# Kernel tuning notes

Measured on AMD Instinct MI355X. Metric: run time of the kernel, lower is better.

The kernel has to match this reference:

```python
import jax, jax.numpy as jnp
import numpy as np

B, C, PC, P = 64, 32, 128, 2048
N = B * C * PC          # 262144 graph nodes
E = 2097152             # ~8 edges per node


def _gcn(x, src, dst, n, W, b):
    # PyG GCNConv: add self loops, sym-normalized mean aggregation of x@W
    xw = x @ W
    sl = jnp.arange(n, dtype=src.dtype)
    s = jnp.concatenate([src, sl]); d = jnp.concatenate([dst, sl])
    deg = jax.ops.segment_sum(jnp.ones(d.shape, xw.dtype), d, num_segments=n)
    dinv = jax.lax.rsqrt(deg)  # deg >= 1 thanks to self loops
    norm = dinv[s] * dinv[d]
    return jax.ops.segment_sum(xw[s] * norm[:, None], d, num_segments=n) + b


def _gat(x, src, dst, n, W, a_src, a_dst, b):
    # PyG GATConv (heads=1): self loops, edge softmax over incoming edges
    xw = x @ W
    sl = jnp.arange(n, dtype=src.dtype)
    s = jnp.concatenate([src, sl]); d = jnp.concatenate([dst, sl])
    e = jax.nn.leaky_relu((xw @ a_src)[s] + (xw @ a_dst)[d], 0.2)
    m = jax.ops.segment_max(jax.lax.stop_gradient(e), d, num_segments=n)
    ex = jnp.exp(e - m[d])
    denom = jax.ops.segment_sum(ex, d, num_segments=n)
    alpha = ex / denom[d]
    return jax.ops.segment_sum(xw[s] * alpha[:, None], d, num_segments=n) + b


def _cross_edges(num_cross, batch_size):
    # faithful to get_c_adjacency: every ordered pair (i!=j) appears twice per graph
    ii, jj = np.meshgrid(np.arange(num_cross), np.arange(num_cross), indexing='ij')
    m = ii != jj
    s, d = ii[m], jj[m]
    s2 = np.concatenate([s, d]); d2 = np.concatenate([d, s])
    off = (np.arange(batch_size) * num_cross)[:, None]
    src = (s2[None] + off).reshape(-1)
    dst = (d2[None] + off).reshape(-1)
    return jnp.asarray(src, jnp.int32), jnp.asarray(dst, jnp.int32)


def _conv1d(x, W, b):
    y = jax.lax.conv_general_dilated(x, W, (2,), ((1, 1),), dimension_numbers=('NCH', 'OIH', 'NCH'))
    return y + b[None, :, None]


def _bn_eval(x, gamma, beta):
    # BatchNorm1d in eval mode with default running stats (mean 0, var 1)
    scale = gamma / np.float32(np.sqrt(1.0 + 1e-5))
    return x * scale[None, :, None] + beta[None, :, None]


def setup_inputs() -> dict:
    key = jax.random.key(0)
    ks = jax.random.split(key, 32)
    rn = lambda k, sh, s=0.1: (jax.random.normal(k, sh, jnp.float32) * s)
    return {
        'x': jax.random.normal(ks[0], (N, 19), jnp.float32),
        'edge_index': jax.random.randint(ks[1], (2, E), 0, N, jnp.int32),
        'points': jax.random.normal(ks[2], (B, 3, P), jnp.float32),
        'W1': rn(ks[3], (19, 32)), 'b1': rn(ks[4], (32,)),
        'W2': rn(ks[5], (32, 64)), 'b2': rn(ks[6], (64,)),
        'W3': rn(ks[7], (64, 64)), 'b3': rn(ks[8], (64,)),
        'Wg1': rn(ks[9], (64, 64)), 'asrc1': rn(ks[10], (64,)), 'adst1': rn(ks[11], (64,)), 'bg1': rn(ks[12], (64,)),
        'Wg2': rn(ks[13], (64, 64)), 'asrc2': rn(ks[14], (64,)), 'adst2': rn(ks[15], (64,)), 'bg2': rn(ks[16], (64,)),
        'c1W': rn(ks[17], (32, 3, 3)), 'c1b': rn(ks[18], (32,)),
        'g1': 1.0 + rn(ks[19], (32,)), 'be1': rn(ks[20], (32,)),
        'c2W': rn(ks[21], (64, 32, 3)), 'c2b': rn(ks[22], (64,)),
        'g2': 1.0 + rn(ks[23], (64,)), 'be2': rn(ks[24], (64,)),
        'c3W': rn(ks[25], (64, 64, 3)), 'c3b': rn(ks[26], (64,)),
        'Wl2': rn(ks[27], (64, 64)), 'bl2': rn(ks[28], (64,)),
        'Wl3': rn(ks[29], (64, 1)), 'bl3': rn(ks[30], (1,)),
        'batch_size': B, 'num_cross': C, 'num_pieces': PC,
    }


def reference(x, edge_index, points, W1, b1, W2, b2, W3, b3,
              Wg1, asrc1, adst1, bg1, Wg2, asrc2, adst2, bg2,
              c1W, c1b, g1, be1, c2W, c2b, g2, be2, c3W, c3b,
              Wl2, bl2, Wl3, bl3, batch_size, num_cross, num_pieces):
    src, dst = edge_index[0], edge_index[1]
    n = x.shape[0]
    h = jax.nn.relu(_gcn(x, src, dst, n, W1, b1))  # dropout is a no-op in eval
    h = jax.nn.leaky_relu(_gcn(h, src, dst, n, W2, b2), 0.01)
    h = jax.nn.leaky_relu(_gcn(h, src, dst, n, W3, b3), 0.01)
    h = _gat(h, src, dst, n, Wg1, asrc1, adst1, bg1)
    h = h.reshape(batch_size, num_cross, num_pieces, -1).mean(-2)  # [B, C, 64]
    s2, d2 = _cross_edges(num_cross, batch_size)
    h = _gat(h.reshape(batch_size * num_cross, 64), s2, d2, batch_size * num_cross, Wg2, asrc2, adst2, bg2)
    h = h.reshape(batch_size, num_cross, 64).mean(1)  # [B, 64]
    p = _bn_eval(jax.nn.leaky_relu(_conv1d(points, c1W, c1b), 0.01), g1, be1)
    p = _bn_eval(jax.nn.leaky_relu(_conv1d(p, c2W, c2b), 0.01), g2, be2)
    p = jax.nn.leaky_relu(_conv1d(p, c3W, c3b), 0.01).mean(-1)  # AdaptiveAvgPool1d(1).squeeze -> [B, 64]
    h = h + p
    h = jax.nn.leaky_relu(h @ Wl2 + bl2, 0.01)
    return jax.nn.sigmoid(h @ Wl3 + bl3)  # [B, 1]
```

## Files before the change

### kernel.cpp

```cpp
#include <hip/hip_runtime.h>
#include <cstdint>
#include <cstddef>

#define NN 262144
#define EE 2097152
#define BB 64
#define CCROSS 32
#define PCC 128
#define PP 2048
#define NBUCK 256
#define BCAP 12288

typedef _Float16 f16;
typedef __attribute__((ext_vector_type(2))) _Float16 f16x2;
typedef __attribute__((ext_vector_type(4))) _Float16 f16x4;
typedef __attribute__((ext_vector_type(8))) _Float16 f16x8;
typedef __attribute__((ext_vector_type(4))) float f32x4;

static __device__ __forceinline__ float lrelu(float x, float s) { return x > 0.f ? x : s * x; }

#if __has_builtin(__builtin_amdgcn_fdot2)
static __device__ __forceinline__ float dot2f(unsigned x, unsigned w, float c) {
    return __builtin_amdgcn_fdot2(__builtin_bit_cast(f16x2, x), __builtin_bit_cast(f16x2, w), c, false);
}
#else
static __device__ __forceinline__ float dot2f(unsigned x, unsigned w, float c) {
    f16x2 a = __builtin_bit_cast(f16x2, x);
    f16x2 b = __builtin_bit_cast(f16x2, w);
    return fmaf((float)a[0], (float)b[0], fmaf((float)a[1], (float)b[1], c));
}
#endif

__global__ __launch_bounds__(256) void bucket_a_k(const int* __restrict__ src, const int* __restrict__ dst,
                                                  unsigned* __restrict__ buckets, int* __restrict__ gcnt) {
    __shared__ int hist[NBUCK];
    __shared__ int base[NBUCK];
    __shared__ unsigned short rankbuf[8192];
    const int tid = threadIdx.x;
    const int e0 = blockIdx.x * 8192;
    hist[tid] = 0;
    __syncthreads();
    for (int i = tid; i < 8192; i += 256) {
        int d = dst[e0 + i];
        rankbuf[i] = (unsigned short)atomicAdd(&hist[d >> 10], 1);
    }
    __syncthreads();
    base[tid] = tid * BCAP + atomicAdd(&gcnt[tid], hist[tid]);
    __syncthreads();
    for (int i = tid; i < 8192; i += 256) {
        int s = src[e0 + i];
        int d = dst[e0 + i];
        int b = d >> 10;
        buckets[base[b] + rankbuf[i]] = ((unsigned)s << 10) | (unsigned)(d & 1023);
    }
}

__global__ void bucket_scan_k(const int* __restrict__ gcnt, int* __restrict__ bbase, int* __restrict__ rp) {
    __shared__ int tmp[256];
    int tid = threadIdx.x;
    int v = gcnt[tid];
    tmp[tid] = v;
    __syncthreads();
    for (int off = 1; off < 256; off <<= 1) {
        int t = (tid >= off) ? tmp[tid - off] : 0;
        __syncthreads();
        tmp[tid] += t;
        __syncthreads();
    }
    bbase[tid] = tmp[tid] - v;
    if (tid == 0) rp[NN] = EE;
}

__global__ __launch_bounds__(256) void bucket_b_k(const unsigned* __restrict__ buckets, const int* __restrict__ gcnt,
                                                  const int* __restrict__ bbase, int* __restrict__ rp,
                                                  float* __restrict__ dinv, int* __restrict__ col) {
    __shared__ int cnt[1024];
    __shared__ int scan[1024];
    __shared__ int wsum[256];
    const int b = blockIdx.x;
    const int tid = threadIdx.x;
    int n = gcnt[b];
    if (n > BCAP) n = BCAP;
    const unsigned* eb = buckets + (size_t)b * BCAP;
    const int gb = bbase[b];
    for (int i = tid; i < 1024; i += 256) cnt[i] = 0;
    __syncthreads();
    for (int i = tid; i < n; i += 256) atomicAdd(&cnt[eb[i] & 1023], 1);
    __syncthreads();
    int b4 = tid * 4;
    int c0 = cnt[b4], c1 = cnt[b4 + 1], c2 = cnt[b4 + 2], c3 = cnt[b4 + 3];
    int tsum = c0 + c1 + c2 + c3;
    wsum[tid] = tsum;
    __syncthreads();
    for (int off = 1; off < 256; off <<= 1) {
        int t = (tid >= off) ? wsum[tid - off] : 0;
        __syncthreads();
        wsum[tid] += t;
        __syncthreads();
    }
    int excl = wsum[tid] - tsum;
    scan[b4] = excl;
    scan[b4 + 1] = excl + c0;
    scan[b4 + 2] = excl + c0 + c1;
    scan[b4 + 3] = excl + c0 + c1 + c2;
    int vbase = b * 1024 + b4;
    rp[vbase + 0] = gb + scan[b4 + 0];
    rp[vbase + 1] = gb + scan[b4 + 1];
    rp[vbase + 2] = gb + scan[b4 + 2];
    rp[vbase + 3] = gb + scan[b4 + 3];
    dinv[vbase + 0] = rsqrtf((float)(c0 + 1));
    dinv[vbase + 1] = rsqrtf((float)(c1 + 1));
    dinv[vbase + 2] = rsqrtf((float)(c2 + 1));
    dinv[vbase + 3] = rsqrtf((float)(c3 + 1));
    __syncthreads();
    for (int i = tid; i < 1024; i += 256) cnt[i] = 0;
    __syncthreads();
    for (int i = tid; i < n; i += 256) {
        unsigned p = eb[i];
        int dl = p & 1023;
        int r = atomicAdd(&cnt[dl], 1);
        col[gb + scan[dl] + r] = (int)(p >> 10);
    }
}

__global__ void zprep_k(const float* __restrict__ x, const float* __restrict__ dinv, f16* __restrict__ z) {
    int v = blockIdx.x * 256 + threadIdx.x;
    if (v >= NN) return;
    float dv = dinv[v];
    const float* xr = x + (size_t)v * 19;
    float vv[20];
#pragma unroll
    for (int k = 0; k < 19; k++) vv[k] = dv * xr[k];
    vv[19] = 0.f;
    f16x4* zr = (f16x4*)(z + (size_t)v * 32);
#pragma unroll
    for (int c = 0; c < 5; c++) {
        f16x4 t = {(f16)vv[4 * c], (f16)vv[4 * c + 1], (f16)vv[4 * c + 2], (f16)vv[4 * c + 3]};
        zr[c] = t;
    }
    f16x4 zz = {(f16)0.f, (f16)0.f, (f16)0.f, (f16)0.f};
#pragma unroll
    for (int c = 5; c < 8; c++) zr[c] = zz;
}

#define ZSTR1 36
template <int KINR, int KOUT, int ACT>
__global__ __launch_bounds__(256) void fused_agg_gemm_k(const f16* __restrict__ z, const int* __restrict__ rp,
                                                        const int* __restrict__ col, const float* __restrict__ Wg,
                                                        const float* __restrict__ dinv, const float* __restrict__ bias,
                                                        f16* __restrict__ zout) {
    constexpr int NO = KOUT / 4;
    __shared__ float Wl[32 * KOUT];
    __shared__ float zrow[64 * ZSTR1];
    const int tid = threadIdx.x;
    for (int i = tid; i < 32 * KOUT; i += 256) Wl[i] = (i < KINR * KOUT) ? Wg[i] : 0.f;

    const int r = tid >> 2;
    const int idx = tid & 3;
    const int v = blockIdx.x * 64 + r;
    const f16x8* z8 = (const f16x8*)z;
    f16x8 a = z8[(size_t)v * 4 + idx];
    float acc8[8];
#pragma unroll
    for (int j = 0; j < 8; j++) acc8[j] = (float)a[j];
    int st = rp[v], e = rp[v + 1];
    int i = st;
    for (; i + 4 <= e; i += 4) {
        int u0 = col[i], u1 = col[i + 1], u2 = col[i + 2], u3 = col[i + 3];
        f16x8 a0 = z8[(size_t)u0 * 4 + idx];
        f16x8 a1 = z8[(size_t)u1 * 4 + idx];
        f16x8 a2 = z8[(size_t)u2 * 4 + idx];
        f16x8 a3 = z8[(size_t)u3 * 4 + idx];
#pragma unroll
        for (int j = 0; j < 8; j++)
            acc8[j] += ((float)a0[j] + (float)a1[j]) + ((float)a2[j] + (float)a3[j]);
    }
    for (; i < e; i++) {
        f16x8 aa = z8[(size_t)col[i] * 4 + idx];
#pragma unroll
        for (int j = 0; j < 8; j++) acc8[j] += (float)aa[j];
    }
    float4 s0, s1;
    s0.x = acc8[0]; s0.y = acc8[1]; s0.z = acc8[2]; s0.w = acc8[3];
    s1.x = acc8[4]; s1.y = acc8[5]; s1.z = acc8[6]; s1.w = acc8[7];
    *(float4*)&zrow[r * ZSTR1 + idx * 8] = s0;
    *(float4*)&zrow[r * ZSTR1 + idx * 8 + 4] = s1;
    __syncthreads();

    float acc[NO];
#pragma unroll
    for (int j = 0; j < NO; j++) acc[j] = 0.f;
#pragma unroll 4
    for (int k = 0; k < 32; k++) {
        float zv = zrow[r * ZSTR1 + k];
        const float* wr = Wl + k * KOUT + NO * idx;
#pragma unroll
        for (int j = 0; j < NO; j++) acc[j] = fmaf(zv, wr[j], acc[j]);
    }
    float dv = dinv[v];
    f16 hv[NO];
#pragma unroll
    for (int j = 0; j < NO; j++) {
        float o = dv * acc[j] + bias[NO * idx + j];
        o = (ACT == 0) ? fmaxf(o, 0.f) : lrelu(o, 0.01f);
        hv[j] = (f16)(o * dv);
    }
    if constexpr (NO == 8) {
        f16x8 h = {hv[0], hv[1], hv[2], hv[3], hv[4], hv[5], hv[6], hv[7]};
        *(f16x8*)(zout + (size_t)v * KOUT + NO * idx) = h;
    } else {
        f16x8 h0 = {hv[0], hv[1], hv[2], hv[3], hv[4], hv[5], hv[6], hv[7]};
        f16x8 h1 = {hv[8], hv[9], hv[10], hv[11], hv[12], hv[13], hv[14], hv[15]};
        f16x8* yo = (f16x8*)(zout + (size_t)v * KOUT + NO * idx);
        yo[0] = h0; yo[1] = h1;
    }
}

__global__ void pack_w_k(const float* __restrict__ W, f16* __restrict__ out) {
    int o = blockIdx.x * 256 + threadIdx.x;
    if (o >= 4096) return;
    int frag = o >> 9;
    int kt = frag >> 2;
    int c = frag & 3;
    int idx = o & 511;
    int l = idx >> 3;
    int j = idx & 7;
    int k = kt * 32 + ((l >> 4) << 3) + j;
    int n = 16 * c + (l & 15);
    out[o] = (f16)W[k * 64 + n];
}

__global__ void pack_c2_k(const float* __restrict__ W, f16* __restrict__ out) {
    int o = blockIdx.x * 256 + threadIdx.x;
    if (o >= 64 * 96) return;
    int ch = o / 96, r = o - ch * 96;
    int k = r >> 5, ci = r & 31;
    out[o] = (f16)W[ch * 96 + ci * 3 + k];
}

__global__ void pack_c3_k(const float* __restrict__ W, f16* __restrict__ out) {
    int o = blockIdx.x * 256 + threadIdx.x;
    if (o >= 64 * 192) return;
    int ch = o / 192, r = o - ch * 192;
    int k = r >> 6, ci = r & 63;
    out[o] = (f16)W[ch * 192 + ci * 3 + k];
}

#define HSTR 72
__global__ __launch_bounds__(256) void gemm3_gat_k(const f16* __restrict__ y, const int* __restrict__ rp,
                                                   const int* __restrict__ col, const f16* __restrict__ w3p,
                                                   const float* __restrict__ dinv, const float* __restrict__ b3,
                                                   const f16* __restrict__ wgp, const float* __restrict__ av,
                                                   const float* __restrict__ ad, f16* __restrict__ xw,
                                                   float* __restrict__ es, float* __restrict__ ed) {
    __shared__ f16 zin[64 * HSTR];
    __shared__ f16 hh[64 * HSTR];
    const int tid = threadIdx.x;
    const int v0 = blockIdx.x * 64;
    {
        const int row = tid >> 2;
        const int idx = tid & 3;
        const int v = v0 + row;
        const f16x8* y8 = (const f16x8*)y;
        f16x8 s0 = y8[(size_t)v * 8 + idx * 2];
        f16x8 s1 = y8[(size_t)v * 8 + idx * 2 + 1];
        float acc[16];
#pragma unroll
        for (int j = 0; j < 8; j++) { acc[j] = (float)s0[j]; acc[8 + j] = (float)s1[j]; }
        int s = rp[v], e = rp[v + 1];
        int i = s;
        for (; i + 4 <= e; i += 4) {
            int u0 = col[i], u1 = col[i + 1], u2 = col[i + 2], u3 = col[i + 3];
            f16x8 a0 = y8[(size_t)u0 * 8 + idx * 2];
            f16x8 a1 = y8[(size_t)u0 * 8 + idx * 2 + 1];
            f16x8 b0 = y8[(size_t)u1 * 8 + idx * 2];
            f16x8 b1 = y8[(size_t)u1 * 8 + idx * 2 + 1];
            f16x8 c0 = y8[(size_t)u2 * 8 + idx * 2];
            f16x8 c1 = y8[(size_t)u2 * 8 + idx * 2 + 1];
            f16x8 d0 = y8[(size_t)u3 * 8 + idx * 2];
            f16x8 d1 = y8[(size_t)u3 * 8 + idx * 2 + 1];
#pragma unroll
            for (int j = 0; j < 8; j++) {
                acc[j] += ((float)a0[j] + (float)b0[j]) + ((float)c0[j] + (float)d0[j]);
                acc[8 + j] += ((float)a1[j] + (float)b1[j]) + ((float)c1[j] + (float)d1[j]);
            }
        }
        for (; i < e; i++) {
            int u = col[i];
            f16x8 a0 = y8[(size_t)u * 8 + idx * 2];
            f16x8 a1 = y8[(size_t)u * 8 + idx * 2 + 1];
#pragma unroll
            for (int j = 0; j < 8; j++) { acc[j] += (float)a0[j]; acc[8 + j] += (float)a1[j]; }
        }
        f16x8 o0, o1;
#pragma unroll
        for (int j = 0; j < 8; j++) { o0[j] = (f16)acc[j]; o1[j] = (f16)acc[8 + j]; }
        *(f16x8*)&zin[row * HSTR + idx * 16] = o0;
        *(f16x8*)&zin[row * HSTR + idx * 16 + 8] = o1;
    }
    __syncthreads();

    const int w = tid >> 6;
    const int l = tid & 63;
    const int m = l & 15;
    const int q = l >> 4;
    const int r0 = 16 * w;

    f32x4 acc0 = {0.f, 0.f, 0.f, 0.f}, acc1 = acc0, acc2 = acc0, acc3 = acc0;
#pragma unroll
    for (int kt = 0; kt < 2; kt++) {
        f16x8 afrag = *(const f16x8*)&zin[(r0 + m) * HSTR + kt * 32 + q * 8];
        f16x8 b0 = *(const f16x8*)&w3p[((kt * 4 + 0) << 9) + l * 8];
        f16x8 b1 = *(const f16x8*)&w3p[((kt * 4 + 1) << 9) + l * 8];
        f16x8 b2 = *(const f16x8*)&w3p[((kt * 4 + 2) << 9) + l * 8];
        f16x8 b3f = *(const f16x8*)&w3p[((kt * 4 + 3) << 9) + l * 8];
        acc0 = __builtin_amdgcn_mfma_f32_16x16x32_f16(afrag, b0, acc0, 0, 0, 0);
        acc1 = __builtin_amdgcn_mfma_f32_16x16x32_f16(afrag, b1, acc1, 0, 0, 0);
        acc2 = __builtin_amdgcn_mfma_f32_16x16x32_f16(afrag, b2, acc2, 0, 0, 0);
        acc3 = __builtin_amdgcn_mfma_f32_16x16x32_f16(afrag, b3f, acc3, 0, 0, 0);
    }
    {
        float dv0 = dinv[v0 + r0 + q * 4 + 0];
        float dv1 = dinv[v0 + r0 + q * 4 + 1];
        float dv2 = dinv[v0 + r0 + q * 4 + 2];
        float dv3 = dinv[v0 + r0 + q * 4 + 3];
#pragma unroll
        for (int c = 0; c < 4; c++) {
            const f32x4* ac = (c == 0) ? &acc0 : (c == 1) ? &acc1 : (c == 2) ? &acc2 : &acc3;
            float bb = b3[16 * c + m];
            hh[(r0 + q * 4 + 0) * HSTR + 16 * c + m] = (f16)lrelu(dv0 * (*ac)[0] + bb, 0.01f);
            hh[(r0 + q * 4 + 1) * HSTR + 16 * c + m] = (f16)lrelu(dv1 * (*ac)[1] + bb, 0.01f);
            hh[(r0 + q * 4 + 2) * HSTR + 16 * c + m] = (f16)lrelu(dv2 * (*ac)[2] + bb, 0.01f);
            hh[(r0 + q * 4 + 3) * HSTR + 16 * c + m] = (f16)lrelu(dv3 * (*ac)[3] + bb, 0.01f);
        }
    }
    __syncthreads();

    acc0 = (f32x4){0.f, 0.f, 0.f, 0.f}; acc1 = acc0; acc2 = acc0; acc3 = acc0;
#pragma unroll
    for (int kt = 0; kt < 2; kt++) {
        f16x8 afrag = *(const f16x8*)&hh[(r0 + m) * HSTR + kt * 32 + q * 8];
        f16x8 b0 = *(const f16x8*)&wgp[((kt * 4 + 0) << 9) + l * 8];
        f16x8 b1 = *(const f16x8*)&wgp[((kt * 4 + 1) << 9) + l * 8];
        f16x8 b2 = *(const f16x8*)&wgp[((kt * 4 + 2) << 9) + l * 8];
        f16x8 b3f = *(const f16x8*)&wgp[((kt * 4 + 3) << 9) + l * 8];
        acc0 = __builtin_amdgcn_mfma_f32_16x16x32_f16(afrag, b0, acc0, 0, 0, 0);
        acc1 = __builtin_amdgcn_mfma_f32_16x16x32_f16(afrag, b1, acc1, 0, 0, 0);
        acc2 = __builtin_amdgcn_mfma_f32_16x16x32_f16(afrag, b2, acc2, 0, 0, 0);
        acc3 = __builtin_amdgcn_mfma_f32_16x16x32_f16(afrag, b3f, acc3, 0, 0, 0);
    }
    {
        float e1[4] = {0.f, 0.f, 0.f, 0.f}, e2[4] = {0.f, 0.f, 0.f, 0.f};
#pragma unroll
        for (int c = 0; c < 4; c++) {
            const f32x4* ac = (c == 0) ? &acc0 : (c == 1) ? &acc1 : (c == 2) ? &acc2 : &acc3;
            float a1 = av[16 * c + m];
            float d1 = ad[16 * c + m];
#pragma unroll
            for (int reg = 0; reg < 4; reg++) {
                float g = (*ac)[reg];
                e1[reg] = fmaf(g, a1, e1[reg]);
                e2[reg] = fmaf(g, d1, e2[reg]);
                xw[(size_t)(v0 + r0 + q * 4 + reg) * 64 + 16 * c + m] = (f16)g;
            }
        }
#pragma unroll
        for (int reg = 0; reg < 4; reg++) {
            e1[reg] += __shfl_xor(e1[reg], 1); e1[reg] += __shfl_xor(e1[reg], 2);
            e1[reg] += __shfl_xor(e1[reg], 4); e1[reg] += __shfl_xor(e1[reg], 8);
            e2[reg] += __shfl_xor(e2[reg], 1); e2[reg] += __shfl_xor(e2[reg], 2);
            e2[reg] += __shfl_xor(e2[reg], 4); e2[reg] += __shfl_xor(e2[reg], 8);
        }
        if (m == 0) {
#pragma unroll
            for (int reg = 0; reg < 4; reg++) {
                es[v0 + r0 + q * 4 + reg] = e1[reg];
                ed[v0 + r0 + q * 4 + reg] = e2[reg];
            }
        }
    }
}

__global__ void gat_w_k(const float* __restrict__ es, const float* __restrict__ ed,
                        const int* __restrict__ rp, const int* __restrict__ col,
                        f16* __restrict__ ewi, float* __restrict__ wsi) {
    int v = blockIdx.x * 256 + threadIdx.x;
    if (v >= NN) return;
    float edv = ed[v];
    float eself = lrelu(es[v] + edv, 0.2f);
    float m = eself;
    int s = rp[v], e = rp[v + 1];
    int i = s;
    float lg[32];
    for (; i + 4 <= e; i += 4) {
        int u0 = col[i], u1 = col[i + 1], u2 = col[i + 2], u3 = col[i + 3];
        float t0 = lrelu(es[u0] + edv, 0.2f);
        float t1 = lrelu(es[u1] + edv, 0.2f);
        float t2 = lrelu(es[u2] + edv, 0.2f);
        float t3 = lrelu(es[u3] + edv, 0.2f);
        int k = i - s;
        if (k + 3 < 32) { lg[k] = t0; lg[k + 1] = t1; lg[k + 2] = t2; lg[k + 3] = t3; }
        m = fmaxf(m, fmaxf(fmaxf(t0, t1), fmaxf(t2, t3)));
    }
    for (; i < e; i++) {
        float t = lrelu(es[col[i]] + edv, 0.2f);
        int k = i - s;
        if (k < 32) lg[k] = t;
        m = fmaxf(m, t);
    }
    float wsl = __expf(eself - m);
    float den = wsl;
    for (i = s; i < e; i++) {
        int k = i - s;
        float t = (k < 32) ? lg[k] : lrelu(es[col[i]] + edv, 0.2f);
        float w = __expf(t - m);
        if (k < 32) lg[k] = w;
        den += w;
    }
    float inv = 1.f / den;
    for (i = s; i < e; i++) {
        int k = i - s;
        float w = (k < 32) ? lg[k] : __expf(lrelu(es[col[i]] + edv, 0.2f) - m);
        ewi[i] = (f16)(w * inv);
    }
    wsi[v] = wsl * inv;
}

__global__ __launch_bounds__(256) void gat_agg_pool_k(const f16* __restrict__ y, const int* __restrict__ rp,
                                                      const int* __restrict__ col, const f16* __restrict__ ewi,
                                                      const float* __restrict__ wsi,
                                                      const float* __restrict__ bias, float* __restrict__ pooled) {
    __shared__ float sred[32 * 68];
    const int g = blockIdx.x;
    const int tid = threadIdx.x;
    const int idx = tid & 7;
    const int slot = tid >> 3;
    const f16x8* y8 = (const f16x8*)y;
    float acc[8];
#pragma unroll
    for (int j = 0; j < 8; j++) acc[j] = 0.f;

#pragma unroll
    for (int pass = 0; pass < 4; pass++) {
        const int v = g * 128 + pass * 32 + slot;
        float ws = wsi[v];
        f16x8 self = y8[(size_t)v * 8 + idx];
#pragma unroll
        for (int j = 0; j < 8; j++) acc[j] = fmaf(ws, (float)self[j], acc[j]);
    }

    const int s = rp[g * 128];
    const int e = rp[g * 128 + 128];
    int i = s + slot;
    for (; i + 96 < e; i += 128) {
        int u0 = col[i], u1 = col[i + 32], u2 = col[i + 64], u3 = col[i + 96];
        float w0 = (float)ewi[i], w1 = (float)ewi[i + 32], w2 = (float)ewi[i + 64], w3 = (float)ewi[i + 96];
        f16x8 a0 = y8[(size_t)u0 * 8 + idx];
        f16x8 a1 = y8[(size_t)u1 * 8 + idx];
        f16x8 a2 = y8[(size_t)u2 * 8 + idx];
        f16x8 a3 = y8[(size_t)u3 * 8 + idx];
#pragma unroll
        for (int j = 0; j < 8; j++)
            acc[j] = fmaf(w0, (float)a0[j], fmaf(w1, (float)a1[j], fmaf(w2, (float)a2[j], fmaf(w3, (float)a3[j], acc[j]))));
    }
    for (; i < e; i += 32) {
        int u = col[i];
        float w = (float)ewi[i];
        f16x8 a = y8[(size_t)u * 8 + idx];
#pragma unroll
        for (int j = 0; j < 8; j++) acc[j] = fmaf(w, (float)a[j], acc[j]);
    }

#pragma unroll
    for (int j = 0; j < 8; j++) sred[slot * 68 + idx * 8 + j] = acc[j];
    __syncthreads();
    if (tid < 64) {
        float s2 = 0.f;
#pragma unroll
        for (int k = 0; k < 32; k++) s2 += sred[k * 68 + tid];
        pooled[(size_t)g * 64 + tid] = s2 * (1.f / 128.f) + bias[tid];
    }
}

__global__ void pool_cross_k(const float* __restrict__ in, float* __restrict__ out) {
    int gid = blockIdx.x * 64 + threadIdx.x;
    if (gid >= BB * 64) return;
    int f = gid & 63, b = gid >> 6;
    const float* p = in + (size_t)b * CCROSS * 64 + f;
    float s = 0.f;
#pragma unroll
    for (int i = 0; i < CCROSS; i++) s += p[(size_t)i * 64];
    out[gid] = s * (1.f / 32.f);
}

template <int KIN, int KOUT>
__global__ void gat_gemm_k(const float* __restrict__ x, const float* __restrict__ W,
                           float* __restrict__ y, const float* __restrict__ av, const float* __restrict__ ad,
                           float* __restrict__ es, float* __restrict__ ed, int n) {
    int v = blockIdx.x * 256 + threadIdx.x;
    if (v >= n) return;
    const float* xr = x + (size_t)v * KIN;
    float acc[KOUT];
#pragma unroll
    for (int j = 0; j < KOUT; j++) acc[j] = 0.f;
#pragma unroll 2
    for (int k = 0; k < KIN; k++) {
        float xv = xr[k];
#pragma unroll
        for (int j = 0; j < KOUT; j++) acc[j] = fmaf(xv, W[k * KOUT + j], acc[j]);
    }
    float e1 = 0.f, e2 = 0.f;
    float4* y4 = (float4*)(y + (size_t)v * KOUT);
#pragma unroll
    for (int j4 = 0; j4 < KOUT / 4; j4++) {
        float4 t;
        t.x = acc[4 * j4 + 0]; t.y = acc[4 * j4 + 1]; t.z = acc[4 * j4 + 2]; t.w = acc[4 * j4 + 3];
        y4[j4] = t;
        e1 = fmaf(t.x, av[4 * j4 + 0], e1); e1 = fmaf(t.y, av[4 * j4 + 1], e1);
        e1 = fmaf(t.z, av[4 * j4 + 2], e1); e1 = fmaf(t.w, av[4 * j4 + 3], e1);
        e2 = fmaf(t.x, ad[4 * j4 + 0], e2); e2 = fmaf(t.y, ad[4 * j4 + 1], e2);
        e2 = fmaf(t.z, ad[4 * j4 + 2], e2); e2 = fmaf(t.w, ad[4 * j4 + 3], e2);
    }
    es[v] = e1; ed[v] = e2;
}

__global__ void cross_att_k(const float* __restrict__ xw, const float* __restrict__ es,
                            const float* __restrict__ ed, const float* __restrict__ bg,
                            float* __restrict__ out) {
    int gid = blockIdx.x * 256 + threadIdx.x;
    if (gid >= BB * CCROSS * 64) return;
    int f = gid & 63;
    int d = (gid >> 6) & 31;
    int g = gid >> 11;
    int base = g * CCROSS;
    float edd = ed[base + d];
    float m = -1e30f;
#pragma unroll
    for (int s = 0; s < CCROSS; s++) {
        float e = lrelu(es[base + s] + edd, 0.2f);
        m = fmaxf(m, e);
    }
    float den = 0.f, acc = 0.f;
#pragma unroll
    for (int s = 0; s < CCROSS; s++) {
        float e = lrelu(es[base + s] + edd, 0.2f);
        float w = __expf(e - m) * ((s == d) ? 1.f : 2.f);
        den += w;
        acc = fmaf(w, xw[(size_t)(base + s) * 64 + f], acc);
    }
    out[gid] = acc / den + bg[f];
}

__global__ __launch_bounds__(256) void conv_fused_k(
        const float* __restrict__ pts, const float* __restrict__ c1W, const float* __restrict__ c1b,
        const float* __restrict__ g1, const float* __restrict__ be1,
        const f16* __restrict__ w2p, const float* __restrict__ c2b,
        const float* __restrict__ g2, const float* __restrict__ be2,
        const f16* __restrict__ w3pc, const float* __restrict__ c3b,
        float* __restrict__ partials) {
    __shared__ __align__(16) float s0[3 * 264];
    __shared__ __align__(16) f16 s1T[132 * 32];
    __shared__ __align__(16) f16 s2T[66 * 64];
    __shared__ float sred[256];

    const int b = blockIdx.x >> 3;
    const int q = blockIdx.x & 7;
    const int tid = threadIdx.x;
    const float bnscale = 0.99999500003749968f;

    const int lo0 = 256 * q - 7;
    for (int t = tid; t < 3 * 263; t += 256) {
        int c = t / 263, j = t - c * 263;
        int p = lo0 + j;
        s0[c * 264 + j] = (p >= 0 && p < PP) ? pts[((size_t)b * 3 + c) * PP + p] : 0.f;
    }
    __syncthreads();

    {
        const int ch = tid & 31;
        const int j0 = tid >> 5;
        float wv[9];
        const float* wg = c1W + ch * 9;
#pragma unroll
        for (int t = 0; t < 9; t++) wv[t] = wg[t];
        const float bs = c1b[ch];
        const float gs = g1[ch] * bnscale;
        const float bt = be1[ch];
        const int lo1 = 128 * q - 3;
        for (int j = j0; j < 131; j += 8) {
            int p1 = lo1 + j;
            float v = 0.f;
            if (p1 >= 0 && p1 < 1024) {
                const float* x0 = s0 + 2 * j;
                float a0 = bs, a1 = 0.f, a2 = 0.f;
#pragma unroll
                for (int c = 0; c < 3; c++) {
                    float2 x01 = *(const float2*)(x0 + c * 264);
                    float x2v = x0[c * 264 + 2];
                    a0 = fmaf(x01.x, wv[c * 3 + 0], a0);
                    a1 = fmaf(x01.y, wv[c * 3 + 1], a1);
                    a2 = fmaf(x2v, wv[c * 3 + 2], a2);
                }
                float acc = a0 + a1 + a2;
                acc = lrelu(acc, 0.01f);
                v = fmaf(acc, gs, bt);
            }
            s1T[j * 32 + ch] = (f16)v;
        }
    }
    __syncthreads();

    {
        const int ch = tid & 63;
        const int jg = tid >> 6;
        unsigned wr[48];
        const uint4* wp = (const uint4*)(w2p + (size_t)ch * 96);
#pragma unroll
        for (int t = 0; t < 12; t++) {
            uint4 u = wp[t];
            wr[4 * t + 0] = u.x; wr[4 * t + 1] = u.y; wr[4 * t + 2] = u.z; wr[4 * t + 3] = u.w;
        }
        const float bs = c2b[ch];
        const float gs = g2[ch] * bnscale;
        const float bt = be2[ch];
        const int lo2v = 64 * q - 1;
        for (int j = jg; j < 65; j += 4) {
            float ak[3] = {bs, 0.f, 0.f};
#pragma unroll
            for (int k = 0; k < 3; k++) {
                const uint4* xp = (const uint4*)(s1T + (2 * j + k) * 32);
                uint4 x0 = xp[0], x1 = xp[1], x2 = xp[2], x3 = xp[3];
                float a = ak[k];
                a = dot2f(x0.x, wr[k * 16 + 0], a);
                a = dot2f(x0.y, wr[k * 16 + 1], a);
                a = dot2f(x0.z, wr[k * 16 + 2], a);
                a = dot2f(x0.w, wr[k * 16 + 3], a);
                a = dot2f(x1.x, wr[k * 16 + 4], a);
                a = dot2f(x1.y, wr[k * 16 + 5], a);
                a = dot2f(x1.z, wr[k * 16 + 6], a);
                a = dot2f(x1.w, wr[k * 16 + 7], a);
                a = dot2f(x2.x, wr[k * 16 + 8], a);
                a = dot2f(x2.y, wr[k * 16 + 9], a);
                a = dot2f(x2.z, wr[k * 16 + 10], a);
                a = dot2f(x2.w, wr[k * 16 + 11], a);
                a = dot2f(x3.x, wr[k * 16 + 12], a);
                a = dot2f(x3.y, wr[k * 16 + 13], a);
                a = dot2f(x3.z, wr[k * 16 + 14], a);
                a = dot2f(x3.w, wr[k * 16 + 15], a);
                ak[k] = a;
            }
            float acc = ak[0] + ak[1] + ak[2];
            int p2 = lo2v + j;
            float v = 0.f;
            if (p2 >= 0 && p2 < 512) v = fmaf(lrelu(acc, 0.01f), gs, bt);
            s2T[j * 64 + ch] = (f16)v;
        }
    }
    __syncthreads();

    {
        const int ch = tid & 63;
        const int jg = tid >> 6;
        unsigned wr[96];
        const uint4* wp = (const uint4*)(w3pc + (size_t)ch * 192);
#pragma unroll
        for (int t = 0; t < 24; t++) {
            uint4 u = wp[t];
            wr[4 * t + 0] = u.x; wr[4 * t + 1] = u.y; wr[4 * t + 2] = u.z; wr[4 * t + 3] = u.w;
        }
        const float bs = c3b[ch];
        float psum = 0.f;
        for (int j = jg; j < 32; j += 4) {
            float ak[3] = {bs, 0.f, 0.f};
#pragma unroll
            for (int k = 0; k < 3; k++) {
                const uint4* xp = (const uint4*)(s2T + (2 * j + k) * 64);
                float a = ak[k];
#pragma unroll
                for (int t = 0; t < 8; t++) {
                    uint4 xv = xp[t];
                    a = dot2f(xv.x, wr[k * 32 + 4 * t + 0], a);
                    a = dot2f(xv.y, wr[k * 32 + 4 * t + 1], a);
                    a = dot2f(xv.z, wr[k * 32 + 4 * t + 2], a);
                    a = dot2f(xv.w, wr[k * 32 + 4 * t + 3], a);
                }
                ak[k] = a;
            }
            psum += lrelu(ak[0] + ak[1] + ak[2], 0.01f);
        }
        sred[tid] = psum;
    }
    __syncthreads();
    if (tid < 64) {
        float s = sred[tid] + sred[tid + 64] + sred[tid + 128] + sred[tid + 192];
        partials[((size_t)b * 8 + q) * 64 + tid] = s;
    }
}

__global__ void head_k(const float* __restrict__ hG, const float* __restrict__ partials,
                       const float* __restrict__ Wl2, const float* __restrict__ bl2,
                       const float* __restrict__ Wl3, const float* __restrict__ bl3,
                       float* __restrict__ out) {
    int b = blockIdx.x;
    int f = threadIdx.x;
    __shared__ float sh[64];
    float p = 0.f;
#pragma unroll
    for (int q = 0; q < 8; q++) p += partials[((size_t)b * 8 + q) * 64 + f];
    float h = hG[b * 64 + f] + p * (1.f / 256.f);
    sh[f] = h;
    __syncthreads();
    float acc = bl2[f];
#pragma unroll
    for (int k = 0; k < 64; k++) acc = fmaf(sh[k], Wl2[k * 64 + f], acc);
    acc = lrelu(acc, 0.01f);
    float pr = acc * Wl3[f];
#pragma unroll
    for (int off = 32; off > 0; off >>= 1) pr += __shfl_down(pr, off, 64);
    if (f == 0) out[b] = 1.f / (1.f + __expf(-(pr + bl3[0])));
}

extern "C" void kernel_launch(void* const* d_in, const int* in_sizes, int n_in,
                              void* d_out, int out_size, void* d_ws, size_t ws_size,
                              hipStream_t stream) {
    const float* x = (const float*)d_in[0];
    const int* ei = (const int*)d_in[1];
    const float* points = (const float*)d_in[2];
    const float* W1 = (const float*)d_in[3];
    const float* b1 = (const float*)d_in[4];
    const float* W2 = (const float*)d_in[5];
    const float* b2 = (const float*)d_in[6];
    const float* W3 = (const float*)d_in[7];
    const float* b3 = (const float*)d_in[8];
    const float* Wg1 = (const float*)d_in[9];
    const float* asrc1 = (const float*)d_in[10];
    const float* adst1 = (const float*)d_in[11];
    const float* bg1 = (const float*)d_in[12];
    const float* Wg2 = (const float*)d_in[13];
    const float* asrc2 = (const float*)d_in[14];
    const float* adst2 = (const float*)d_in[15];
    const float* bg2 = (const float*)d_in[16];
    const float* c1W = (const float*)d_in[17];
    const float* c1b = (const float*)d_in[18];
    const float* g1 = (const float*)d_in[19];
    const float* be1 = (const float*)d_in[20];
    const float* c2W = (const float*)d_in[21];
    const float* c2b = (const float*)d_in[22];
    const float* g2 = (const float*)d_in[23];
    const float* be2 = (const float*)d_in[24];
    const float* c3W = (const float*)d_in[25];
    const float* c3b = (const float*)d_in[26];
    const float* Wl2 = (const float*)d_in[27];
    const float* bl2 = (const float*)d_in[28];
    const float* Wl3 = (const float*)d_in[29];
    const float* bl3 = (const float*)d_in[30];

    const int* src = ei;
    const int* dst = ei + EE;

    char* w = (char*)d_ws;
    size_t off = 0;
    auto A = [&](size_t bytes) -> void* {
        void* p = w + off;
        off = (off + bytes + 255) & ~(size_t)255;
        return p;
    };
    int* colb = (int*)A((size_t)EE * 4);
    int* rp = (int*)A((size_t)(NN + 1) * 4);
    int* gcnt = (int*)A(NBUCK * 4);
    int* bbase = (int*)A(NBUCK * 4);
    float* dinv = (float*)A((size_t)NN * 4);
    float* bufA = (float*)A((size_t)NN * 64 * 4);
    f16* bufH1 = (f16*)A((size_t)NN * 64 * 2);
    f16* bufH2 = (f16*)A((size_t)NN * 64 * 2);
    f16* ewi = (f16*)A((size_t)EE * 2);
    float* wsi = (float*)A((size_t)NN * 4);
    float* es = (float*)A((size_t)NN * 4);
    float* edv = (float*)A((size_t)NN * 4);
    f16* w3p = (f16*)A(4096 * 2);
    f16* wgp = (f16*)A(4096 * 2);
    f16* wc2p = (f16*)A(64 * 96 * 2);
    f16* wc3p = (f16*)A(64 * 192 * 2);
    float* pooled = (float*)A((size_t)BB * CCROSS * 64 * 4);
    float* xw2 = (float*)A((size_t)BB * CCROSS * 64 * 4);
    float* es2 = (float*)A((size_t)BB * CCROSS * 4);
    float* ed2 = (float*)A((size_t)BB * CCROSS * 4);
    float* crosso = (float*)A((size_t)BB * CCROSS * 64 * 4);
    float* hG = (float*)A((size_t)BB * 64 * 4);
    float* partials = (float*)A((size_t)BB * 8 * 64 * 4);

    unsigned* buckets = (unsigned*)bufA;

    hipMemsetAsync(gcnt, 0, NBUCK * 4, stream);
    bucket_a_k<<<EE / 8192, 256, 0, stream>>>(src, dst, buckets, gcnt);
    bucket_scan_k<<<1, 256, 0, stream>>>(gcnt, bbase, rp);
    bucket_b_k<<<NBUCK, 256, 0, stream>>>(buckets, gcnt, bbase, rp, dinv, colb);

    pack_c2_k<<<24, 256, 0, stream>>>(c2W, wc2p);
    pack_c3_k<<<48, 256, 0, stream>>>(c3W, wc3p);
    conv_fused_k<<<BB * 8, 256, 0, stream>>>(points, c1W, c1b, g1, be1, wc2p, c2b, g2, be2, wc3p, c3b, partials);
    pack_w_k<<<16, 256, 0, stream>>>(W3, w3p);
    pack_w_k<<<16, 256, 0, stream>>>(Wg1, wgp);

    zprep_k<<<NN / 256, 256, 0, stream>>>(x, dinv, bufH1);
    fused_agg_gemm_k<19, 32, 0><<<NN / 64, 256, 0, stream>>>(bufH1, rp, colb, W1, dinv, b1, bufH2);
    fused_agg_gemm_k<32, 64, 1><<<NN / 64, 256, 0, stream>>>(bufH2, rp, colb, W2, dinv, b2, bufH1);
    gemm3_gat_k<<<NN / 64, 256, 0, stream>>>(bufH1, rp, colb, w3p, dinv, b3, wgp, asrc1, adst1,
                                             bufH2, es, edv);

    gat_w_k<<<NN / 256, 256, 0, stream>>>(es, edv, rp, colb, ewi, wsi);
    gat_agg_pool_k<<<BB * CCROSS, 256, 0, stream>>>(bufH2, rp, colb, ewi, wsi, bg1, pooled);

    gat_gemm_k<64, 64><<<(BB * CCROSS) / 256, 256, 0, stream>>>(pooled, Wg2, xw2, asrc2, adst2, es2, ed2, BB * CCROSS);
    cross_att_k<<<(BB * CCROSS * 64) / 256, 256, 0, stream>>>(xw2, es2, ed2, bg2, crosso);
    pool_cross_k<<<BB, 64, 0, stream>>>(crosso, hG);

    head_k<<<BB, 64, 0, stream>>>(hG, partials, Wl2, bl2, Wl3, bl3, (float*)d_out);
}
```

Before: 480.4 us.

## Fuse small launches: scan into bucket pass, GAT weights into pooling, cross-GAT into head

```diff
diff --git a/kernel.cpp b/kernel.cpp
--- a/kernel.cpp
+++ b/kernel.cpp
@@ -55,34 +55,29 @@
     }
 }
 
-__global__ void bucket_scan_k(const int* __restrict__ gcnt, int* __restrict__ bbase, int* __restrict__ rp) {
-    __shared__ int tmp[256];
-    int tid = threadIdx.x;
-    int v = gcnt[tid];
-    tmp[tid] = v;
-    __syncthreads();
-    for (int off = 1; off < 256; off <<= 1) {
-        int t = (tid >= off) ? tmp[tid - off] : 0;
-        __syncthreads();
-        tmp[tid] += t;
-        __syncthreads();
-    }
-    bbase[tid] = tmp[tid] - v;
-    if (tid == 0) rp[NN] = EE;
-}
-
 __global__ __launch_bounds__(256) void bucket_b_k(const unsigned* __restrict__ buckets, const int* __restrict__ gcnt,
-                                                  const int* __restrict__ bbase, int* __restrict__ rp,
+                                                  int* __restrict__ rp,
                                                   float* __restrict__ dinv, int* __restrict__ col) {
     __shared__ int cnt[1024];
     __shared__ int scan[1024];
     __shared__ int wsum[256];
     const int b = blockIdx.x;
     const int tid = threadIdx.x;
+
+    wsum[tid] = gcnt[tid];
+    __syncthreads();
+    for (int off = 1; off < 256; off <<= 1) {
+        int t = (tid >= off) ? wsum[tid - off] : 0;
+        __syncthreads();
+        wsum[tid] += t;
+        __syncthreads();
+    }
+    const int gb = wsum[b] - gcnt[b];
+    if (b == 0 && tid == 0) rp[NN] = EE;
+
     int n = gcnt[b];
     if (n > BCAP) n = BCAP;
     const unsigned* eb = buckets + (size_t)b * BCAP;
-    const int gb = bbase[b];
     for (int i = tid; i < 1024; i += 256) cnt[i] = 0;
     __syncthreads();
     for (int i = tid; i < n; i += 256) atomicAdd(&cnt[eb[i] & 1023], 1);
@@ -216,34 +211,35 @@
     }
 }
 
-__global__ void pack_w_k(const float* __restrict__ W, f16* __restrict__ out) {
+__global__ void pack_all_k(const float* __restrict__ W3, const float* __restrict__ Wg1,
+                           const float* __restrict__ c2W, const float* __restrict__ c3W,
+                           f16* __restrict__ w3p, f16* __restrict__ wgp,
+                           f16* __restrict__ wc2p, f16* __restrict__ wc3p) {
     int o = blockIdx.x * 256 + threadIdx.x;
-    if (o >= 4096) return;
-    int frag = o >> 9;
-    int kt = frag >> 2;
-    int c = frag & 3;
-    int idx = o & 511;
-    int l = idx >> 3;
-    int j = idx & 7;
-    int k = kt * 32 + ((l >> 4) << 3) + j;
-    int n = 16 * c + (l & 15);
-    out[o] = (f16)W[k * 64 + n];
-}
-
-__global__ void pack_c2_k(const float* __restrict__ W, f16* __restrict__ out) {
-    int o = blockIdx.x * 256 + threadIdx.x;
-    if (o >= 64 * 96) return;
-    int ch = o / 96, r = o - ch * 96;
-    int k = r >> 5, ci = r & 31;
-    out[o] = (f16)W[ch * 96 + ci * 3 + k];
-}
-
-__global__ void pack_c3_k(const float* __restrict__ W, f16* __restrict__ out) {
-    int o = blockIdx.x * 256 + threadIdx.x;
-    if (o >= 64 * 192) return;
-    int ch = o / 192, r = o - ch * 192;
-    int k = r >> 6, ci = r & 63;
-    out[o] = (f16)W[ch * 192 + ci * 3 + k];
+    if (o < 8192) {
+        int oo = o & 4095;
+        const float* W = (o < 4096) ? W3 : Wg1;
+        f16* out = (o < 4096) ? w3p : wgp;
+        int frag = oo >> 9;
+        int kt = frag >> 2;
+        int c = frag & 3;
+        int idx = oo & 511;
+        int l = idx >> 3;
+        int j = idx & 7;
+        int k = kt * 32 + ((l >> 4) << 3) + j;
+        int n = 16 * c + (l & 15);
+        out[oo] = (f16)W[k * 64 + n];
+    } else if (o < 14336) {
+        int oo = o - 8192;
+        int ch = oo / 96, r = oo - ch * 96;
+        int k = r >> 5, ci = r & 31;
+        wc2p[oo] = (f16)c2W[ch * 96 + ci * 3 + k];
+    } else if (o < 26624) {
+        int oo = o - 14336;
+        int ch = oo / 192, r = oo - ch * 192;
+        int k = r >> 6, ci = r & 63;
+        wc3p[oo] = (f16)c3W[ch * 192 + ci * 3 + k];
+    }
 }
 
 #define HSTR 72
@@ -381,58 +377,56 @@
     }
 }
 
-__global__ void gat_w_k(const float* __restrict__ es, const float* __restrict__ ed,
-                        const int* __restrict__ rp, const int* __restrict__ col,
-                        f16* __restrict__ ewi, float* __restrict__ wsi) {
-    int v = blockIdx.x * 256 + threadIdx.x;
-    if (v >= NN) return;
-    float edv = ed[v];
-    float eself = lrelu(es[v] + edv, 0.2f);
-    float m = eself;
-    int s = rp[v], e = rp[v + 1];
-    int i = s;
-    float lg[32];
-    for (; i + 4 <= e; i += 4) {
-        int u0 = col[i], u1 = col[i + 1], u2 = col[i + 2], u3 = col[i + 3];
-        float t0 = lrelu(es[u0] + edv, 0.2f);
-        float t1 = lrelu(es[u1] + edv, 0.2f);
-        float t2 = lrelu(es[u2] + edv, 0.2f);
-        float t3 = lrelu(es[u3] + edv, 0.2f);
-        int k = i - s;
-        if (k + 3 < 32) { lg[k] = t0; lg[k + 1] = t1; lg[k + 2] = t2; lg[k + 3] = t3; }
-        m = fmaxf(m, fmaxf(fmaxf(t0, t1), fmaxf(t2, t3)));
-    }
-    for (; i < e; i++) {
-        float t = lrelu(es[col[i]] + edv, 0.2f);
-        int k = i - s;
-        if (k < 32) lg[k] = t;
-        m = fmaxf(m, t);
-    }
-    float wsl = __expf(eself - m);
-    float den = wsl;
-    for (i = s; i < e; i++) {
-        int k = i - s;
-        float t = (k < 32) ? lg[k] : lrelu(es[col[i]] + edv, 0.2f);
-        float w = __expf(t - m);
-        if (k < 32) lg[k] = w;
-        den += w;
-    }
-    float inv = 1.f / den;
-    for (i = s; i < e; i++) {
-        int k = i - s;
-        float w = (k < 32) ? lg[k] : __expf(lrelu(es[col[i]] + edv, 0.2f) - m);
-        ewi[i] = (f16)(w * inv);
-    }
-    wsi[v] = wsl * inv;
-}
-
-__global__ __launch_bounds__(256) void gat_agg_pool_k(const f16* __restrict__ y, const int* __restrict__ rp,
-                                                      const int* __restrict__ col, const f16* __restrict__ ewi,
-                                                      const float* __restrict__ wsi,
-                                                      const float* __restrict__ bias, float* __restrict__ pooled) {
+__global__ __launch_bounds__(256) void gat_aggw_pool_k(const f16* __restrict__ y, const int* __restrict__ rp,
+                                                       const int* __restrict__ col,
+                                                       const float* __restrict__ es, const float* __restrict__ ed,
+                                                       const float* __restrict__ bias, f16* __restrict__ ewg,
+                                                       float* __restrict__ pooled) {
     __shared__ float sred[32 * 68];
+    __shared__ f16 ewl[2048];
+    __shared__ float wsl[128];
+    __shared__ int rpl[129];
     const int g = blockIdx.x;
     const int tid = threadIdx.x;
+    for (int t = tid; t < 129; t += 256) rpl[t] = rp[g * 128 + t];
+    __syncthreads();
+    const int sG = rpl[0], eG = rpl[128];
+    const bool ovf = (eG - sG) > 2048;
+
+    if (tid < 128) {
+        const int v = g * 128 + tid;
+        const int s = rpl[tid], e = rpl[tid + 1];
+        float edv = ed[v];
+        float eself = lrelu(es[v] + edv, 0.2f);
+        float m = eself;
+        float lg[32];
+        for (int i = s; i < e; i++) {
+            float t = lrelu(es[col[i]] + edv, 0.2f);
+            int k = i - s;
+            if (k < 32) lg[k] = t;
+            m = fmaxf(m, t);
+        }
+        float wv = __expf(eself - m);
+        float den = wv;
+        for (int i = s; i < e; i++) {
+            int k = i - s;
+            float t = (k < 32) ? lg[k] : lrelu(es[col[i]] + edv, 0.2f);
+            float w = __expf(t - m);
+            if (k < 32) lg[k] = w;
+            den += w;
+        }
+        float inv = 1.f / den;
+        for (int i = s; i < e; i++) {
+            int k = i - s;
+            float w = (k < 32) ? lg[k] : __expf(lrelu(es[col[i]] + edv, 0.2f) - m);
+            f16 wh = (f16)(w * inv);
+            int off = i - sG;
+            if (off < 2048) ewl[off] = wh; else ewg[i] = wh;
+        }
+        wsl[tid] = wv * inv;
+    }
+    __syncthreads();
+
     const int idx = tid & 7;
     const int slot = tid >> 3;
     const f16x8* y8 = (const f16x8*)y;
@@ -443,32 +437,41 @@
 #pragma unroll
     for (int pass = 0; pass < 4; pass++) {
         const int v = g * 128 + pass * 32 + slot;
-        float ws = wsi[v];
+        float ws = wsl[pass * 32 + slot];
         f16x8 self = y8[(size_t)v * 8 + idx];
 #pragma unroll
         for (int j = 0; j < 8; j++) acc[j] = fmaf(ws, (float)self[j], acc[j]);
     }
 
-    const int s = rp[g * 128];
-    const int e = rp[g * 128 + 128];
-    int i = s + slot;
-    for (; i + 96 < e; i += 128) {
-        int u0 = col[i], u1 = col[i + 32], u2 = col[i + 64], u3 = col[i + 96];
-        float w0 = (float)ewi[i], w1 = (float)ewi[i + 32], w2 = (float)ewi[i + 64], w3 = (float)ewi[i + 96];
-        f16x8 a0 = y8[(size_t)u0 * 8 + idx];
-        f16x8 a1 = y8[(size_t)u1 * 8 + idx];
-        f16x8 a2 = y8[(size_t)u2 * 8 + idx];
-        f16x8 a3 = y8[(size_t)u3 * 8 + idx];
-#pragma unroll
-        for (int j = 0; j < 8; j++)
-            acc[j] = fmaf(w0, (float)a0[j], fmaf(w1, (float)a1[j], fmaf(w2, (float)a2[j], fmaf(w3, (float)a3[j], acc[j]))));
-    }
-    for (; i < e; i += 32) {
-        int u = col[i];
-        float w = (float)ewi[i];
-        f16x8 a = y8[(size_t)u * 8 + idx];
-#pragma unroll
-        for (int j = 0; j < 8; j++) acc[j] = fmaf(w, (float)a[j], acc[j]);
+    if (!ovf) {
+        int i = sG + slot;
+        for (; i + 96 < eG; i += 128) {
+            int o = i - sG;
+            int u0 = col[i], u1 = col[i + 32], u2 = col[i + 64], u3 = col[i + 96];
+            float w0 = (float)ewl[o], w1 = (float)ewl[o + 32], w2 = (float)ewl[o + 64], w3 = (float)ewl[o + 96];
+            f16x8 a0 = y8[(size_t)u0 * 8 + idx];
+            f16x8 a1 = y8[(size_t)u1 * 8 + idx];
+            f16x8 a2 = y8[(size_t)u2 * 8 + idx];
+            f16x8 a3 = y8[(size_t)u3 * 8 + idx];
+#pragma unroll
+            for (int j = 0; j < 8; j++)
+                acc[j] = fmaf(w0, (float)a0[j], fmaf(w1, (float)a1[j], fmaf(w2, (float)a2[j], fmaf(w3, (float)a3[j], acc[j]))));
+        }
+        for (; i < eG; i += 32) {
+            int u = col[i];
+            float w = (float)ewl[i - sG];
+            f16x8 a = y8[(size_t)u * 8 + idx];
+#pragma unroll
+            for (int j = 0; j < 8; j++) acc[j] = fmaf(w, (float)a[j], acc[j]);
+        }
+    } else {
+        for (int i = sG + slot; i < eG; i += 32) {
+            int o = i - sG;
+            float w = (float)((o < 2048) ? ewl[o] : ewg[i]);
+            f16x8 a = y8[(size_t)col[i] * 8 + idx];
+#pragma unroll
+            for (int j = 0; j < 8; j++) acc[j] = fmaf(w, (float)a[j], acc[j]);
+        }
     }
 
 #pragma unroll
@@ -482,73 +485,95 @@
     }
 }
 
-__global__ void pool_cross_k(const float* __restrict__ in, float* __restrict__ out) {
-    int gid = blockIdx.x * 64 + threadIdx.x;
-    if (gid >= BB * 64) return;
-    int f = gid & 63, b = gid >> 6;
-    const float* p = in + (size_t)b * CCROSS * 64 + f;
-    float s = 0.f;
-#pragma unroll
-    for (int i = 0; i < CCROSS; i++) s += p[(size_t)i * 64];
-    out[gid] = s * (1.f / 32.f);
-}
-
-template <int KIN, int KOUT>
-__global__ void gat_gemm_k(const float* __restrict__ x, const float* __restrict__ W,
-                           float* __restrict__ y, const float* __restrict__ av, const float* __restrict__ ad,
-                           float* __restrict__ es, float* __restrict__ ed, int n) {
-    int v = blockIdx.x * 256 + threadIdx.x;
-    if (v >= n) return;
-    const float* xr = x + (size_t)v * KIN;
-    float acc[KOUT];
-#pragma unroll
-    for (int j = 0; j < KOUT; j++) acc[j] = 0.f;
-#pragma unroll 2
-    for (int k = 0; k < KIN; k++) {
-        float xv = xr[k];
-#pragma unroll
-        for (int j = 0; j < KOUT; j++) acc[j] = fmaf(xv, W[k * KOUT + j], acc[j]);
-    }
-    float e1 = 0.f, e2 = 0.f;
-    float4* y4 = (float4*)(y + (size_t)v * KOUT);
-#pragma unroll
-    for (int j4 = 0; j4 < KOUT / 4; j4++) {
-        float4 t;
-        t.x = acc[4 * j4 + 0]; t.y = acc[4 * j4 + 1]; t.z = acc[4 * j4 + 2]; t.w = acc[4 * j4 + 3];
-        y4[j4] = t;
-        e1 = fmaf(t.x, av[4 * j4 + 0], e1); e1 = fmaf(t.y, av[4 * j4 + 1], e1);
-        e1 = fmaf(t.z, av[4 * j4 + 2], e1); e1 = fmaf(t.w, av[4 * j4 + 3], e1);
-        e2 = fmaf(t.x, ad[4 * j4 + 0], e2); e2 = fmaf(t.y, ad[4 * j4 + 1], e2);
-        e2 = fmaf(t.z, ad[4 * j4 + 2], e2); e2 = fmaf(t.w, ad[4 * j4 + 3], e2);
-    }
-    es[v] = e1; ed[v] = e2;
-}
-
-__global__ void cross_att_k(const float* __restrict__ xw, const float* __restrict__ es,
-                            const float* __restrict__ ed, const float* __restrict__ bg,
-                            float* __restrict__ out) {
-    int gid = blockIdx.x * 256 + threadIdx.x;
-    if (gid >= BB * CCROSS * 64) return;
-    int f = gid & 63;
-    int d = (gid >> 6) & 31;
-    int g = gid >> 11;
-    int base = g * CCROSS;
-    float edd = ed[base + d];
-    float m = -1e30f;
-#pragma unroll
-    for (int s = 0; s < CCROSS; s++) {
-        float e = lrelu(es[base + s] + edd, 0.2f);
-        m = fmaxf(m, e);
-    }
-    float den = 0.f, acc = 0.f;
-#pragma unroll
-    for (int s = 0; s < CCROSS; s++) {
-        float e = lrelu(es[base + s] + edd, 0.2f);
-        float w = __expf(e - m) * ((s == d) ? 1.f : 2.f);
-        den += w;
-        acc = fmaf(w, xw[(size_t)(base + s) * 64 + f], acc);
-    }
-    out[gid] = acc / den + bg[f];
+__global__ __launch_bounds__(256) void cross_head_k(const float* __restrict__ pooled, const float* __restrict__ Wg2,
+                                                    const float* __restrict__ asrc2, const float* __restrict__ adst2,
+                                                    const float* __restrict__ bg2, const float* __restrict__ partials,
+                                                    const float* __restrict__ Wl2, const float* __restrict__ bl2,
+                                                    const float* __restrict__ Wl3, const float* __restrict__ bl3,
+                                                    float* __restrict__ out) {
+    __shared__ float pl[32 * 64];
+    __shared__ float wl[64 * 64];
+    __shared__ float xw2[32 * 64];
+    __shared__ float es2[32], ed2[32];
+    __shared__ float hsum[4][64];
+    __shared__ float hbuf[64];
+    const int b = blockIdx.x;
+    const int tid = threadIdx.x;
+
+    for (int t = tid; t < 2048; t += 256) pl[t] = pooled[(size_t)b * 2048 + t];
+    for (int t = tid; t < 4096; t += 256) wl[t] = Wg2[t];
+    __syncthreads();
+
+    {
+        const int f = tid & 63;
+        const int n0 = tid >> 6;
+#pragma unroll
+        for (int pass = 0; pass < 8; pass++) {
+            int n = n0 + 4 * pass;
+            float acc = 0.f;
+#pragma unroll 8
+            for (int k = 0; k < 64; k++) acc = fmaf(pl[n * 64 + k], wl[k * 64 + f], acc);
+            xw2[n * 64 + f] = acc;
+        }
+    }
+    __syncthreads();
+    if (tid < 32) {
+        float e1 = 0.f, e2 = 0.f;
+#pragma unroll 8
+        for (int k = 0; k < 64; k++) {
+            float v = xw2[tid * 64 + k];
+            e1 = fmaf(v, asrc2[k], e1);
+            e2 = fmaf(v, adst2[k], e2);
+        }
+        es2[tid] = e1; ed2[tid] = e2;
+    }
+    __syncthreads();
+
+    {
+        const int f = tid & 63;
+        const int dg = tid >> 6;
+        float psum = 0.f;
+#pragma unroll 1
+        for (int pass = 0; pass < 8; pass++) {
+            int d = dg + 4 * pass;
+            float edd = ed2[d];
+            float m = -1e30f;
+#pragma unroll
+            for (int s = 0; s < 32; s++) m = fmaxf(m, lrelu(es2[s] + edd, 0.2f));
+            float den = 0.f, acc = 0.f;
+#pragma unroll
+            for (int s = 0; s < 32; s++) {
+                float e = lrelu(es2[s] + edd, 0.2f);
+                float w = __expf(e - m) * ((s == d) ? 1.f : 2.f);
+                den += w;
+                acc = fmaf(w, xw2[s * 64 + f], acc);
+            }
+            psum += acc / den;
+        }
+        hsum[dg][f] = psum;
+    }
+    __syncthreads();
+
+    if (tid < 64) {
+        const int f = tid;
+        float hc = (hsum[0][f] + hsum[1][f] + hsum[2][f] + hsum[3][f]) * (1.f / 32.f) + bg2[f];
+        float p = 0.f;
+#pragma unroll
+        for (int q = 0; q < 8; q++) p += partials[((size_t)b * 8 + q) * 64 + f];
+        hbuf[f] = hc + p * (1.f / 256.f);
+    }
+    __syncthreads();
+    if (tid < 64) {
+        const int f = tid;
+        float acc = bl2[f];
+#pragma unroll 8
+        for (int k = 0; k < 64; k++) acc = fmaf(hbuf[k], Wl2[k * 64 + f], acc);
+        acc = lrelu(acc, 0.01f);
+        float pr = acc * Wl3[f];
+#pragma unroll
+        for (int off = 32; off > 0; off >>= 1) pr += __shfl_down(pr, off, 64);
+        if (f == 0) out[b] = 1.f / (1.f + __expf(-(pr + bl3[0])));
+    }
 }
 
 __global__ __launch_bounds__(256) void conv_fused_k(
@@ -695,29 +720,6 @@
         float s = sred[tid] + sred[tid + 64] + sred[tid + 128] + sred[tid + 192];
         partials[((size_t)b * 8 + q) * 64 + tid] = s;
     }
-}
-
-__global__ void head_k(const float* __restrict__ hG, const float* __restrict__ partials,
-                       const float* __restrict__ Wl2, const float* __restrict__ bl2,
-                       const float* __restrict__ Wl3, const float* __restrict__ bl3,
-                       float* __restrict__ out) {
-    int b = blockIdx.x;
-    int f = threadIdx.x;
-    __shared__ float sh[64];
-    float p = 0.f;
-#pragma unroll
-    for (int q = 0; q < 8; q++) p += partials[((size_t)b * 8 + q) * 64 + f];
-    float h = hG[b * 64 + f] + p * (1.f / 256.f);
-    sh[f] = h;
-    __syncthreads();
-    float acc = bl2[f];
-#pragma unroll
-    for (int k = 0; k < 64; k++) acc = fmaf(sh[k], Wl2[k * 64 + f], acc);
-    acc = lrelu(acc, 0.01f);
-    float pr = acc * Wl3[f];
-#pragma unroll
-    for (int off = 32; off > 0; off >>= 1) pr += __shfl_down(pr, off, 64);
-    if (f == 0) out[b] = 1.f / (1.f + __expf(-(pr + bl3[0])));
 }
 
 extern "C" void kernel_launch(void* const* d_in, const int* in_sizes, int n_in,
@@ -768,13 +770,11 @@
     int* colb = (int*)A((size_t)EE * 4);
     int* rp = (int*)A((size_t)(NN + 1) * 4);
     int* gcnt = (int*)A(NBUCK * 4);
-    int* bbase = (int*)A(NBUCK * 4);
     float* dinv = (float*)A((size_t)NN * 4);
     float* bufA = (float*)A((size_t)NN * 64 * 4);
     f16* bufH1 = (f16*)A((size_t)NN * 64 * 2);
     f16* bufH2 = (f16*)A((size_t)NN * 64 * 2);
     f16* ewi = (f16*)A((size_t)EE * 2);
-    float* wsi = (float*)A((size_t)NN * 4);
     float* es = (float*)A((size_t)NN * 4);
     float* edv = (float*)A((size_t)NN * 4);
     f16* w3p = (f16*)A(4096 * 2);
@@ -782,25 +782,16 @@
     f16* wc2p = (f16*)A(64 * 96 * 2);
     f16* wc3p = (f16*)A(64 * 192 * 2);
     float* pooled = (float*)A((size_t)BB * CCROSS * 64 * 4);
-    float* xw2 = (float*)A((size_t)BB * CCROSS * 64 * 4);
-    float* es2 = (float*)A((size_t)BB * CCROSS * 4);
-    float* ed2 = (float*)A((size_t)BB * CCROSS * 4);
-    float* crosso = (float*)A((size_t)BB * CCROSS * 64 * 4);
-    float* hG = (float*)A((size_t)BB * 64 * 4);
     float* partials = (float*)A((size_t)BB * 8 * 64 * 4);
 
     unsigned* buckets = (unsigned*)bufA;
 
     hipMemsetAsync(gcnt, 0, NBUCK * 4, stream);
     bucket_a_k<<<EE / 8192, 256, 0, stream>>>(src, dst, buckets, gcnt);
-    bucket_scan_k<<<1, 256, 0, stream>>>(gcnt, bbase, rp);
-    bucket_b_k<<<NBUCK, 256, 0, stream>>>(buckets, gcnt, bbase, rp, dinv, colb);
-
-    pack_c2_k<<<24, 256, 0, stream>>>(c2W, wc2p);
-    pack_c3_k<<<48, 256, 0, stream>>>(c3W, wc3p);
+    bucket_b_k<<<NBUCK, 256, 0, stream>>>(buckets, gcnt, rp, dinv, colb);
+
+    pack_all_k<<<104, 256, 0, stream>>>(W3, Wg1, c2W, c3W, w3p, wgp, wc2p, wc3p);
     conv_fused_k<<<BB * 8, 256, 0, stream>>>(points, c1W, c1b, g1, be1, wc2p, c2b, g2, be2, wc3p, c3b, partials);
-    pack_w_k<<<16, 256, 0, stream>>>(W3, w3p);
-    pack_w_k<<<16, 256, 0, stream>>>(Wg1, wgp);
 
     zprep_k<<<NN / 256, 256, 0, stream>>>(x, dinv, bufH1);
     fused_agg_gemm_k<19, 32, 0><<<NN / 64, 256, 0, stream>>>(bufH1, rp, colb, W1, dinv, b1, bufH2);
@@ -808,12 +799,8 @@
     gemm3_gat_k<<<NN / 64, 256, 0, stream>>>(bufH1, rp, colb, w3p, dinv, b3, wgp, asrc1, adst1,
                                              bufH2, es, edv);
 
-    gat_w_k<<<NN / 256, 256, 0, stream>>>(es, edv, rp, colb, ewi, wsi);
-    gat_agg_pool_k<<<BB * CCROSS, 256, 0, stream>>>(bufH2, rp, colb, ewi, wsi, bg1, pooled);
-
-    gat_gemm_k<64, 64><<<(BB * CCROSS) / 256, 256, 0, stream>>>(pooled, Wg2, xw2, asrc2, adst2, es2, ed2, BB * CCROSS);
-    cross_att_k<<<(BB * CCROSS * 64) / 256, 256, 0, stream>>>(xw2, es2, ed2, bg2, crosso);
-    pool_cross_k<<<BB, 64, 0, stream>>>(crosso, hG);
-
-    head_k<<<BB, 64, 0, stream>>>(hG, partials, Wl2, bl2, Wl3, bl3, (float*)d_out);
-}
+    gat_aggw_pool_k<<<BB * CCROSS, 256, 0, stream>>>(bufH2, rp, colb, es, edv, bg1, ewi, pooled);
+
+    cross_head_k<<<BB, 256, 0, stream>>>(pooled, Wg2, asrc2, adst2, bg2, partials,
+                                         Wl2, bl2, Wl3, bl3, (float*)d_out);
+}
```

Measured after the change: 461.9 us. 3.9% less time.
